# Performance work log

Measured on AMD Instinct MI355X. Metric: run time of the kernel, lower is better.

The kernel has to match this reference:

```python
import jax, jax.numpy as jnp
import numpy as np

LN_EPS = 1e-5
SUM_CLAMP = 1e-12


def setup_inputs() -> dict:
    key = jax.random.key(0)
    ks = jax.random.split(key, 10)
    L, D, H, P, E = 200000, 512, 512, 16384, 200000
    lesion_x = jax.random.normal(ks[0], (L, D), dtype=jnp.float32)
    edge_index = jnp.stack([
        jax.random.randint(ks[1], (E,), 0, P),   # patient idx
        jax.random.randint(ks[2], (E,), 0, L),   # lesion idx
    ], axis=0).astype(jnp.int64)
    s1 = 1.0 / np.sqrt(D)
    s2 = 1.0 / np.sqrt(H)
    W1 = jax.random.uniform(ks[3], (H, D), jnp.float32, -s1, s1)
    b1 = jax.random.uniform(ks[4], (H,), jnp.float32, -s1, s1)
    W2 = jax.random.uniform(ks[5], (1, H), jnp.float32, -s2, s2)
    b2 = jax.random.uniform(ks[6], (1,), jnp.float32, -s2, s2)
    Wp = jax.random.uniform(ks[7], (768, D), jnp.float32, -s1, s1)
    bp = jax.random.uniform(ks[8], (768,), jnp.float32, -s1, s1)
    gamma = jnp.ones((768,), jnp.float32)
    beta = jnp.zeros((768,), jnp.float32)
    return dict(lesion_x=lesion_x, patient_to_lesion_edge_index=edge_index,
                num_patients_in_batch=P, W1=W1, b1=b1, W2=W2, b2=b2,
                Wp=Wp, bp=bp, gamma=gamma, beta=beta)


def reference(lesion_x, patient_to_lesion_edge_index, num_patients_in_batch,
              W1, b1, W2, b2, Wp, bp, gamma, beta):
    P = int(num_patients_in_batch)
    pat = patient_to_lesion_edge_index[0]
    les = patient_to_lesion_edge_index[1]
    feats = lesion_x[les]                                  # [E, D] gather
    h = jnp.tanh(feats @ W1.T + b1)                        # [E, H]
    scores = (h @ W2.T + b2)[:, 0]                         # [E]
    smax = jax.ops.segment_max(scores, pat, num_segments=P)  # [P]
    ex = jnp.exp(scores - smax[pat])                       # [E]
    esum = jax.ops.segment_sum(ex, pat, num_segments=P)
    esum = jnp.maximum(esum, SUM_CLAMP)
    alpha = ex / esum[pat]                                 # [E]
    agg = jax.ops.segment_sum(feats * alpha[:, None], pat, num_segments=P)  # [P, D]
    proj = agg @ Wp.T + bp                                 # [P, 768]
    mu = jnp.mean(proj, axis=-1, keepdims=True)
    var = jnp.mean(jnp.square(proj - mu), axis=-1, keepdims=True)
    out = (proj - mu) * jax.lax.rsqrt(var + LN_EPS) * gamma + beta
    return out
```

## Files before the change

kernel.cpp:

```cpp
#include <hip/hip_runtime.h>
#include <hip/hip_bf16.h>

#define D_DIM 512
#define H_DIM 512
#define O_DIM 768

using bf16x8 = __attribute__((ext_vector_type(8))) short;
using f32x4  = __attribute__((ext_vector_type(4))) float;

static __device__ __forceinline__ unsigned cvtpk(float lo, float hi){
  unsigned r;
  asm("v_cvt_pk_bf16_f32 %0, %1, %2" : "=v"(r) : "v"(lo), "v"(hi));
  return r;
}

static __device__ __forceinline__ float bflo(unsigned u){
  return __uint_as_float(u << 16);
}
static __device__ __forceinline__ float bfhi(unsigned u){
  return __uint_as_float(u & 0xffff0000u);
}

static __device__ __forceinline__ float fast_tanh(float x){
  float e = __expf(2.f * x);
  return 1.f - 2.f / (e + 1.f);
}

static __device__ __forceinline__ unsigned f2ord(float f){
  unsigned u = __float_as_uint(f);
  return (u & 0x80000000u) ? ~u : (u | 0x80000000u);
}
static __device__ __forceinline__ float ord2f(unsigned u){
  u = (u & 0x80000000u) ? (u & 0x7fffffffu) : ~u;
  return __uint_as_float(u);
}

static __device__ __forceinline__ void gload16(const void* g, void* l){
  __builtin_amdgcn_global_load_lds(
      (const __attribute__((address_space(1))) void*)g,
      (__attribute__((address_space(3))) void*)l, 16, 0, 0);
}

__global__ void cvt_bf16(const float* __restrict__ in,
                         unsigned short* __restrict__ out, int n8)
{
  int stride = gridDim.x * blockDim.x;
  for (int i = blockIdx.x*blockDim.x + threadIdx.x; i < n8; i += stride){
    const float4* p = (const float4*)in + (size_t)i*2;
    float4 a = p[0], b = p[1];
    uint4 pk;
    pk.x = cvtpk(a.x, a.y);
    pk.y = cvtpk(a.z, a.w);
    pk.z = cvtpk(b.x, b.y);
    pk.w = cvtpk(b.z, b.w);
    ((uint4*)out)[i] = pk;
  }
}

__launch_bounds__(256, 2)
__global__ void gemm1_wide(const float* __restrict__ A,
                           const short* __restrict__ Bm,
                           const float* __restrict__ bias,
                           const float* __restrict__ w2,
                           float* __restrict__ out,
                           short* __restrict__ Ab,
                           int M, int nwg)
{
  __shared__ short lds_a[128*64];
  __shared__ short lds_b[256*64];

  const int q  = nwg >> 3, rr = nwg & 7;
  const int xcd = blockIdx.x & 7, bidx = blockIdx.x >> 3;
  const int swz = (xcd < rr ? xcd*(q+1) : rr*(q+1) + (xcd-rr)*q) + bidx;
  const int colBase = (swz & 1) * 256;
  const int rowBase = (swz >> 1) * 128;
  const bool writeAb = (colBase == 0);

  const int tid  = threadIdx.x;
  const int lane = tid & 63;
  const int w    = tid >> 6;
  const int wr   = w >> 1, wc = w & 1;
  const int lr   = lane & 15;
  const int lk   = lane >> 4;

  const int srow = tid >> 4;
  const int sgf  = tid & 15;
  const int rlocB = lane >> 3;
  const int jB    = lane & 7;

  f32x4 acc[4][8];
  #pragma unroll
  for (int i = 0; i < 4; ++i)
    #pragma unroll
    for (int j = 0; j < 8; ++j)
      acc[i][j] = (f32x4){0.f, 0.f, 0.f, 0.f};

  for (int kt = 0; kt < 512/64; ++kt){
    const int kOff = kt * 64;
    float4 va[8];
    #pragma unroll
    for (int c = 0; c < 8; ++c){
      int gA = rowBase + c*16 + srow; if (gA > M-1) gA = M-1;
      va[c] = *(const float4*)(A + (size_t)gA*512 + kOff + sgf*4);
    }
    #pragma unroll
    for (int c = 0; c < 8; ++c){
      int rt = w*64 + c*8 + rlocB;
      int js = jB ^ (rt & 7);
      gload16(Bm + (size_t)(colBase + rt)*512 + kOff + js*8,
              &lds_b[(w*64 + c*8)*64]);
    }
    #pragma unroll
    for (int c = 0; c < 8; ++c){
      int rt = c*16 + srow;
      uint2 pk = { cvtpk(va[c].x, va[c].y), cvtpk(va[c].z, va[c].w) };
      int sidx = (rt*64 + sgf*4) ^ ((rt & 7) << 3);
      *(uint2*)&lds_a[sidx] = pk;
      if (writeAb){
        int gA = rowBase + rt;
        if (gA < M) *(uint2*)(Ab + (size_t)gA*512 + kOff + sgf*4) = pk;
      }
    }
    __syncthreads();
    #pragma unroll
    for (int kk = 0; kk < 2; ++kk){
      bf16x8 af[4], bfr[8];
      #pragma unroll
      for (int mf = 0; mf < 4; ++mf){
        int r   = wr*64 + mf*16 + lr;
        int idx = (r*64 + kk*32 + lk*8) ^ ((r & 7) << 3);
        af[mf] = *(bf16x8*)&lds_a[idx];
      }
      #pragma unroll
      for (int nf = 0; nf < 8; ++nf){
        int r   = wc*128 + nf*16 + lr;
        int idx = (r*64 + kk*32 + lk*8) ^ ((r & 7) << 3);
        bfr[nf] = *(bf16x8*)&lds_b[idx];
      }
      __builtin_amdgcn_s_setprio(1);
      #pragma unroll
      for (int mf = 0; mf < 4; ++mf)
        #pragma unroll
        for (int nf = 0; nf < 8; ++nf)
          acc[mf][nf] = __builtin_amdgcn_mfma_f32_16x16x32_bf16(
              af[mf], bfr[nf], acc[mf][nf], 0, 0, 0);
      __builtin_amdgcn_s_setprio(0);
    }
    __syncthreads();
  }

  #pragma unroll
  for (int mf = 0; mf < 4; ++mf){
    float part[4] = {0.f,0.f,0.f,0.f};
    #pragma unroll
    for (int nf = 0; nf < 8; ++nf){
      int gc = colBase + wc*128 + nf*16 + lr;
      float b = bias[gc], wv = w2[gc];
      #pragma unroll
      for (int r = 0; r < 4; ++r)
        part[r] += fast_tanh(acc[mf][nf][r] + b) * wv;
    }
    #pragma unroll
    for (int r = 0; r < 4; ++r){
      part[r] += __shfl_xor(part[r], 1);
      part[r] += __shfl_xor(part[r], 2);
      part[r] += __shfl_xor(part[r], 4);
      part[r] += __shfl_xor(part[r], 8);
    }
    if (lr == 0){
      int gr = rowBase + wr*64 + mf*16 + lk*4;
      #pragma unroll
      for (int r = 0; r < 4; ++r)
        if (gr + r < M) atomicAdd(&out[gr + r], part[r]);
    }
  }
}

__launch_bounds__(256, 2)
__global__ void gemm2_bf16(const short* __restrict__ A,
                           const short* __restrict__ Bm,
                           const float* __restrict__ bias,
                           float* __restrict__ out,
                           int M, int outStride)
{
  __shared__ short lds_a[128*64];
  __shared__ short lds_b[128*64];

  const int tid  = threadIdx.x;
  const int lane = tid & 63;
  const int w    = tid >> 6;
  const int wr   = w >> 1, wc = w & 1;
  const int lr   = lane & 15;
  const int lk   = lane >> 4;

  const int colBase = blockIdx.x * 128;
  const int rowBase = blockIdx.y * 128;

  f32x4 acc[4][4];
  #pragma unroll
  for (int i = 0; i < 4; ++i)
    #pragma unroll
    for (int j = 0; j < 4; ++j)
      acc[i][j] = (f32x4){0.f, 0.f, 0.f, 0.f};

  const int subrow = lane >> 3;
  const int gpre   = lane & 7;

  for (int kt = 0; kt < 512/64; ++kt){
    const int kOff = kt * 64;
    #pragma unroll
    for (int c = 0; c < 4; ++c){
      int r    = w*32 + c*8 + subrow;
      int gran = gpre ^ (r & 7);
      int gA   = rowBase + r; if (gA > M-1) gA = M-1;
      gload16(A  + (size_t)gA*512 + kOff + gran*8, &lds_a[(w*32 + c*8)*64]);
      int gB   = colBase + r;
      gload16(Bm + (size_t)gB*512 + kOff + gran*8, &lds_b[(w*32 + c*8)*64]);
    }
    __syncthreads();
    #pragma unroll
    for (int kk = 0; kk < 2; ++kk){
      bf16x8 af[4], bfr[4];
      #pragma unroll
      for (int mf = 0; mf < 4; ++mf){
        int r   = wr*64 + mf*16 + lr;
        int idx = (r*64 + kk*32 + lk*8) ^ ((r & 7) << 3);
        af[mf] = *(bf16x8*)&lds_a[idx];
      }
      #pragma unroll
      for (int nf = 0; nf < 4; ++nf){
        int r   = wc*64 + nf*16 + lr;
        int idx = (r*64 + kk*32 + lk*8) ^ ((r & 7) << 3);
        bfr[nf] = *(bf16x8*)&lds_b[idx];
      }
      #pragma unroll
      for (int mf = 0; mf < 4; ++mf)
        #pragma unroll
        for (int nf = 0; nf < 4; ++nf)
          acc[mf][nf] = __builtin_amdgcn_mfma_f32_16x16x32_bf16(
              af[mf], bfr[nf], acc[mf][nf], 0, 0, 0);
    }
    __syncthreads();
  }

  #pragma unroll
  for (int mf = 0; mf < 4; ++mf){
    int gr = rowBase + wr*64 + mf*16 + lk*4;
    #pragma unroll
    for (int nf = 0; nf < 4; ++nf){
      int gc = colBase + wc*64 + nf*16 + lr;
      float b = bias[gc];
      #pragma unroll
      for (int r = 0; r < 4; ++r)
        if (gr + r < M) out[(size_t)(gr + r)*outStride + gc] = acc[mf][nf][r] + b;
    }
  }
}

__global__ void edge_pass1(const int* __restrict__ edge, int E,
                           const float* __restrict__ scores,
                           unsigned* __restrict__ smax_o,
                           int* __restrict__ hist)
{
  int e = blockIdx.x*256 + threadIdx.x;
  if (e >= E) return;
  int p = edge[e], l = edge[E + e];
  atomicMax(&smax_o[p], f2ord(scores[l]));
  atomicAdd(&hist[p], 1);
}

__global__ void scan_kernel(const int* __restrict__ hist,
                            int* __restrict__ offsets, int P)
{
  __shared__ int s[1024];
  int t = threadIdx.x;
  int local[16]; int sum = 0;
  #pragma unroll
  for (int i = 0; i < 16; ++i){
    int idx = t*16 + i;
    local[i] = (idx < P) ? hist[idx] : 0;
    sum += local[i];
  }
  s[t] = sum;
  __syncthreads();
  for (int off = 1; off < 1024; off <<= 1){
    int v = (t >= off) ? s[t - off] : 0;
    __syncthreads();
    s[t] += v;
    __syncthreads();
  }
  int run = s[t] - sum;
  #pragma unroll
  for (int i = 0; i < 16; ++i){
    int idx = t*16 + i;
    if (idx < P) offsets[idx] = run;
    run += local[i];
  }
}

__global__ void edge_pass2(const int* __restrict__ edge, int E,
                           const float* __restrict__ scores,
                           const unsigned* __restrict__ smax_o,
                           float* __restrict__ ex,
                           float* __restrict__ esum,
                           const int* __restrict__ offsets,
                           int* __restrict__ cursor,
                           int* __restrict__ sorted)
{
  int e = blockIdx.x*256 + threadIdx.x;
  if (e >= E) return;
  int p = edge[e], l = edge[E + e];
  float v = __expf(scores[l] - ord2f(smax_o[p]));
  ex[e] = v;
  atomicAdd(&esum[p], v);
  int pos = atomicAdd(&cursor[p], 1);
  sorted[offsets[p] + pos] = e;
}

__global__ void agg_kernel(const int* __restrict__ edge, int E,
                           const short* __restrict__ Ab,
                           const float* __restrict__ ex,
                           const float* __restrict__ esum,
                           const int* __restrict__ offsets,
                           const int* __restrict__ hist,
                           const int* __restrict__ sorted,
                           unsigned* __restrict__ aggb)
{
  int p    = blockIdx.x*4 + (threadIdx.x >> 6);
  int lane = threadIdx.x & 63;
  int n = hist[p];
  if (n == 0) return;
  int start = offsets[p];
  float inv = 1.f / fmaxf(esum[p], 1e-12f);
  float a[8] = {0.f,0.f,0.f,0.f,0.f,0.f,0.f,0.f};
  int e0 = sorted[start];
  uint4 u = *(const uint4*)(Ab + (size_t)edge[E + e0]*512 + lane*8);
  float alpha = ex[e0] * inv;
  for (int i = 0; i < n; ++i){
    uint4 uc = u; float ac = alpha;
    if (i + 1 < n){
      int e2 = sorted[start + i + 1];
      u = *(const uint4*)(Ab + (size_t)edge[E + e2]*512 + lane*8);
      alpha = ex[e2] * inv;
    }
    a[0] += ac * bflo(uc.x);  a[1] += ac * bfhi(uc.x);
    a[2] += ac * bflo(uc.y);  a[3] += ac * bfhi(uc.y);
    a[4] += ac * bflo(uc.z);  a[5] += ac * bfhi(uc.z);
    a[6] += ac * bflo(uc.w);  a[7] += ac * bfhi(uc.w);
  }
  uint4 o = { cvtpk(a[0],a[1]), cvtpk(a[2],a[3]),
              cvtpk(a[4],a[5]), cvtpk(a[6],a[7]) };
  *(uint4*)&aggb[(size_t)p*256 + lane*4] = o;
}

__global__ void ln_kernel(float* __restrict__ out,
                          const float* __restrict__ gamma,
                          const float* __restrict__ beta)
{
  __shared__ float red1[4];
  __shared__ float red2[4];
  int p = blockIdx.x;
  float* row = out + (size_t)p*768;
  int t = threadIdx.x;
  float v0 = row[t], v1 = row[t+256], v2 = row[t+512];
  float s = v0 + v1 + v2;
  #pragma unroll
  for (int off = 32; off; off >>= 1) s += __shfl_down(s, off);
  int lane = t & 63, wv = t >> 6;
  if (lane == 0) red1[wv] = s;
  __syncthreads();
  float mean = (red1[0]+red1[1]+red1[2]+red1[3]) * (1.f/768.f);
  float d0 = v0-mean, d1 = v1-mean, d2 = v2-mean;
  float qq = d0*d0 + d1*d1 + d2*d2;
  #pragma unroll
  for (int off = 32; off; off >>= 1) qq += __shfl_down(qq, off);
  if (lane == 0) red2[wv] = qq;
  __syncthreads();
  float var = (red2[0]+red2[1]+red2[2]+red2[3]) * (1.f/768.f);
  float inv = rsqrtf(var + 1e-5f);
  row[t]     = d0*inv*gamma[t]     + beta[t];
  row[t+256] = d1*inv*gamma[t+256] + beta[t+256];
  row[t+512] = d2*inv*gamma[t+512] + beta[t+512];
}

extern "C" void kernel_launch(void* const* d_in, const int* in_sizes, int n_in,
                              void* d_out, int out_size, void* d_ws, size_t ws_size,
                              hipStream_t stream)
{
  const float* lesion_x = (const float*)d_in[0];
  const int*   edge     = (const int*)d_in[1];
  const float* W1    = (const float*)d_in[3];
  const float* b1    = (const float*)d_in[4];
  const float* W2    = (const float*)d_in[5];
  const float* Wp    = (const float*)d_in[7];
  const float* bp    = (const float*)d_in[8];
  const float* gamma = (const float*)d_in[9];
  const float* beta  = (const float*)d_in[10];

  const int L = in_sizes[0] / D_DIM;
  const int E = in_sizes[1] / 2;
  const int P = out_size / O_DIM;

  auto al = [](size_t x){ return (x + 255) & ~(size_t)255; };
  char* ws = (char*)d_ws;
  size_t oScores = 0;
  size_t oSmax   = oScores + al((size_t)L*4);
  size_t oEsum   = oSmax   + al((size_t)P*4);
  size_t oHist   = oEsum   + al((size_t)P*4);
  size_t oCursor = oHist   + al((size_t)P*4);
  size_t smallEnd= oCursor + al((size_t)P*4);
  size_t oAggB   = smallEnd;
  size_t aggEnd  = oAggB   + al((size_t)P*D_DIM*2);
  size_t oOff    = aggEnd;
  size_t oEx     = oOff    + al((size_t)P*4);
  size_t oSorted = oEx     + al((size_t)E*4);
  size_t oW1b    = oSorted + al((size_t)E*4);
  size_t oWpb    = oW1b    + al((size_t)H_DIM*D_DIM*2);
  size_t oAb     = oWpb    + al((size_t)O_DIM*D_DIM*2);
  size_t need    = oAb     + al((size_t)L*D_DIM*2);
  (void)need;

  float*    scores = (float*)(ws + oScores);
  unsigned* smax_o = (unsigned*)(ws + oSmax);
  float*    esum   = (float*)(ws + oEsum);
  int*      hist   = (int*)(ws + oHist);
  int*      cursor = (int*)(ws + oCursor);
  unsigned* aggb   = (unsigned*)(ws + oAggB);
  int*      offs   = (int*)(ws + oOff);
  float*    ex     = (float*)(ws + oEx);
  int*      sorted = (int*)(ws + oSorted);
  short*    W1b    = (short*)(ws + oW1b);
  short*    Wpb    = (short*)(ws + oWpb);
  short*    Ab     = (short*)(ws + oAb);

  hipMemsetAsync(d_ws, 0, smallEnd, stream);
  hipMemsetAsync(ws + oAggB, 0, (size_t)P*D_DIM*2, stream);

  dim3 b256(256);
  int eb = (E + 255) / 256;

  cvt_bf16<<<128, b256, 0, stream>>>(W1, (unsigned short*)W1b, H_DIM*D_DIM/8);
  cvt_bf16<<<192, b256, 0, stream>>>(Wp, (unsigned short*)Wpb, O_DIM*D_DIM/8);

  int nRow = (L + 127) / 128;
  int nwg  = 2 * nRow;
  gemm1_wide<<<nwg, b256, 0, stream>>>(lesion_x, W1b, b1, W2, scores, Ab, L, nwg);

  edge_pass1<<<eb, b256, 0, stream>>>(edge, E, scores, smax_o, hist);
  scan_kernel<<<1, 1024, 0, stream>>>(hist, offs, P);
  edge_pass2<<<eb, b256, 0, stream>>>(edge, E, scores, smax_o, ex, esum,
                                      offs, cursor, sorted);
  agg_kernel<<<P/4, b256, 0, stream>>>(edge, E, Ab, ex, esum, offs,
                                       hist, sorted, aggb);
  gemm2_bf16<<<dim3(O_DIM/128, P/128), b256, 0, stream>>>(
      (const short*)aggb, Wpb, bp, (float*)d_out, P, O_DIM);
  ln_kernel<<<P, b256, 0, stream>>>((float*)d_out, gamma, beta);
}
```

Before: 439.2 us.

## Compute full 512-column hidden tile per block and reduce scores in LDS

The first GEMM now uses 512-thread blocks that each cover 128 rows and all 512 hidden columns, instead of two 256-thread blocks splitting the columns. Each lesion row is read and converted once, and the tanh·w2 partials are reduced through shared memory and written directly, so the per-row atomics, the XCD swizzle and the zeroing of the scores buffer are no longer needed. The cost is a larger shared-memory footprint (64 KB for B plus A), which may lower occupancy, and fewer blocks in the grid.

New measurement: 440.9 us. Within noise of the previous version (+0.4%).

```diff
diff --git a/kernel.cpp b/kernel.cpp
--- a/kernel.cpp
+++ b/kernel.cpp
@@ -57,31 +57,26 @@
   }
 }
 
-__launch_bounds__(256, 2)
-__global__ void gemm1_wide(const float* __restrict__ A,
+__launch_bounds__(512, 2)
+__global__ void gemm1_full(const float* __restrict__ A,
                            const short* __restrict__ Bm,
                            const float* __restrict__ bias,
                            const float* __restrict__ w2,
-                           float* __restrict__ out,
+                           float* __restrict__ scores,
                            short* __restrict__ Ab,
-                           int M, int nwg)
+                           int M)
 {
   __shared__ short lds_a[128*64];
-  __shared__ short lds_b[256*64];
-
-  const int q  = nwg >> 3, rr = nwg & 7;
-  const int xcd = blockIdx.x & 7, bidx = blockIdx.x >> 3;
-  const int swz = (xcd < rr ? xcd*(q+1) : rr*(q+1) + (xcd-rr)*q) + bidx;
-  const int colBase = (swz & 1) * 256;
-  const int rowBase = (swz >> 1) * 128;
-  const bool writeAb = (colBase == 0);
+  __shared__ short lds_b[512*64];
 
   const int tid  = threadIdx.x;
   const int lane = tid & 63;
   const int w    = tid >> 6;
-  const int wr   = w >> 1, wc = w & 1;
+  const int wr   = w >> 2;
+  const int wc   = w & 3;
   const int lr   = lane & 15;
   const int lk   = lane >> 4;
+  const int rowBase = blockIdx.x * 128;
 
   const int srow = tid >> 4;
   const int sgf  = tid & 15;
@@ -95,31 +90,28 @@
     for (int j = 0; j < 8; ++j)
       acc[i][j] = (f32x4){0.f, 0.f, 0.f, 0.f};
 
-  for (int kt = 0; kt < 512/64; ++kt){
+  for (int kt = 0; kt < 8; ++kt){
     const int kOff = kt * 64;
-    float4 va[8];
-    #pragma unroll
-    for (int c = 0; c < 8; ++c){
-      int gA = rowBase + c*16 + srow; if (gA > M-1) gA = M-1;
+    float4 va[4];
+    #pragma unroll
+    for (int c = 0; c < 4; ++c){
+      int gA = rowBase + c*32 + srow; if (gA > M-1) gA = M-1;
       va[c] = *(const float4*)(A + (size_t)gA*512 + kOff + sgf*4);
     }
     #pragma unroll
     for (int c = 0; c < 8; ++c){
       int rt = w*64 + c*8 + rlocB;
       int js = jB ^ (rt & 7);
-      gload16(Bm + (size_t)(colBase + rt)*512 + kOff + js*8,
-              &lds_b[(w*64 + c*8)*64]);
-    }
-    #pragma unroll
-    for (int c = 0; c < 8; ++c){
-      int rt = c*16 + srow;
+      gload16(Bm + (size_t)rt*512 + kOff + js*8, &lds_b[(w*64 + c*8)*64]);
+    }
+    #pragma unroll
+    for (int c = 0; c < 4; ++c){
+      int rt = c*32 + srow;
       uint2 pk = { cvtpk(va[c].x, va[c].y), cvtpk(va[c].z, va[c].w) };
       int sidx = (rt*64 + sgf*4) ^ ((rt & 7) << 3);
       *(uint2*)&lds_a[sidx] = pk;
-      if (writeAb){
-        int gA = rowBase + rt;
-        if (gA < M) *(uint2*)(Ab + (size_t)gA*512 + kOff + sgf*4) = pk;
-      }
+      int gA = rowBase + rt;
+      if (gA < M) *(uint2*)(Ab + (size_t)gA*512 + kOff + sgf*4) = pk;
     }
     __syncthreads();
     #pragma unroll
@@ -149,12 +141,13 @@
     __syncthreads();
   }
 
+  float* red = (float*)lds_a;
   #pragma unroll
   for (int mf = 0; mf < 4; ++mf){
     float part[4] = {0.f,0.f,0.f,0.f};
     #pragma unroll
     for (int nf = 0; nf < 8; ++nf){
-      int gc = colBase + wc*128 + nf*16 + lr;
+      int gc = wc*128 + nf*16 + lr;
       float b = bias[gc], wv = w2[gc];
       #pragma unroll
       for (int r = 0; r < 4; ++r)
@@ -168,11 +161,18 @@
       part[r] += __shfl_xor(part[r], 8);
     }
     if (lr == 0){
-      int gr = rowBase + wr*64 + mf*16 + lk*4;
-      #pragma unroll
-      for (int r = 0; r < 4; ++r)
-        if (gr + r < M) atomicAdd(&out[gr + r], part[r]);
-    }
+      #pragma unroll
+      for (int r = 0; r < 4; ++r){
+        int row = wr*64 + mf*16 + lk*4 + r;
+        red[row*4 + wc] = part[r];
+      }
+    }
+  }
+  __syncthreads();
+  if (tid < 128){
+    int gr = rowBase + tid;
+    if (gr < M)
+      scores[gr] = red[tid*4] + red[tid*4+1] + red[tid*4+2] + red[tid*4+3];
   }
 }
 
@@ -433,7 +433,7 @@
   short*    Wpb    = (short*)(ws + oWpb);
   short*    Ab     = (short*)(ws + oAb);
 
-  hipMemsetAsync(d_ws, 0, smallEnd, stream);
+  hipMemsetAsync(ws + oSmax, 0, smallEnd - oSmax, stream);
   hipMemsetAsync(ws + oAggB, 0, (size_t)P*D_DIM*2, stream);
 
   dim3 b256(256);
@@ -443,8 +443,8 @@
   cvt_bf16<<<192, b256, 0, stream>>>(Wp, (unsigned short*)Wpb, O_DIM*D_DIM/8);
 
   int nRow = (L + 127) / 128;
-  int nwg  = 2 * nRow;
-  gemm1_wide<<<nwg, b256, 0, stream>>>(lesion_x, W1b, b1, W2, scores, Ab, L, nwg);
+  gemm1_full<<<nRow, dim3(512), 0, stream>>>(lesion_x, W1b, b1, W2,
+                                             scores, Ab, L);
 
   edge_pass1<<<eb, b256, 0, stream>>>(edge, E, scores, smax_o, hist);
   scan_kernel<<<1, 1024, 0, stream>>>(hist, offs, P);
```
